# Performance work log

Hardware: AMD Instinct MI355X
Metric: run time of the kernel (lower is better)

The kernel has to match this reference:

```python
import jax, jax.numpy as jnp
import numpy as np

B, T, IN = 8, 1000, 80
CONV = 256
CCEP = 222            # ltv_out_channels
FFT_SIZE = 1024
HOP = 256
WIN = 2 * HOP         # 512
PAD = (FFT_SIZE - CCEP) // 2   # 401
NFFT = 2048


def _conv1d_same(x, W, b, groups):
    # x: (B,T,C); W: (O, C//groups, 3); equivalent to torch Conv1d pad=2 then [1:-1]
    y = jax.lax.conv_general_dilated(
        jnp.transpose(x, (0, 2, 1)), W, (1,), [(1, 1)],
        feature_group_count=groups,
        dimension_numbers=('NCH', 'OIH', 'NCH'))
    return jnp.transpose(y, (0, 2, 1)) + b


def _forward(x, z, W1, b1, W2, b2, W3, b3, W4, b4):
    Bx, Tx, _ = x.shape
    # ---- ConvLayers ----
    h = jax.nn.relu(_conv1d_same(x, W1, b1, 1))
    h = jax.nn.relu(_conv1d_same(h, W2, b2, 8))
    h = jax.nn.relu(_conv1d_same(h, W3, b3, 8))
    ccep = _conv1d_same(h, W4, b4, 1)            # (B,T,222)
    q = jnp.arange(1, CCEP // 2 + 1, dtype=x.dtype)
    quef = jnp.concatenate([q[::-1], q])          # [111..1,1..111]
    ccep = ccep / quef
    # ---- ccep -> impulse (log-magnitude cepstrum -> minimum-ish phase impulse) ----
    c = jnp.pad(ccep, ((0, 0), (0, 0), (PAD, PAD)))           # (B,T,1024)
    Y = jnp.fft.fft(c, n=FFT_SIZE, axis=-1)
    mag = jnp.power(10.0, Y.real)
    imp = jnp.fft.ifft(mag * jnp.exp(1j * Y.imag), n=FFT_SIZE, axis=-1).real  # (B,T,1024)
    # ---- time-varying impulse convolution (cross-correlation per frame) ----
    L = z.shape[-1]
    zz = z.reshape(Bx, 1, L)
    zp = jnp.pad(zz, ((0, 0), (0, 0), (WIN // 2 - 1, WIN // 2)))
    starts = jnp.arange(Tx) * HOP
    frames = zp[:, :, starts[:, None] + jnp.arange(WIN)]       # (B,1,T,512)
    fp = jnp.pad(frames, ((0, 0), (0, 0), (0, 0), (FFT_SIZE // 2 - 1, FFT_SIZE // 2)))  # len 1535
    # corr[s] = sum_k fp[s+k] * imp[k], s in [0,512); linear corr via zero-padded FFT
    Fz = jnp.fft.rfft(fp, n=NFFT, axis=-1)                     # (B,1,T,NFFT//2+1)
    Fy = jnp.fft.rfft(imp, n=NFFT, axis=-1)[:, None]           # (B,1,T,NFFT//2+1)
    corr = jnp.fft.irfft(Fz * jnp.conj(Fy), n=NFFT, axis=-1)[..., :WIN]  # (B,1,T,512)
    # ---- overlap-add ----
    n = jnp.arange(WIN, dtype=x.dtype)
    win = 0.5 * (1.0 - jnp.cos(2.0 * jnp.pi * n / WIN))        # periodic hann, win_norm=1
    zw = corr * win
    l, r = zw[..., :HOP], zw[..., HOP:]
    out = l + jnp.roll(r, 1, axis=2)
    return out.reshape(Bx, 1, Tx * HOP)


def setup_inputs() -> dict:
    key = jax.random.key(0)
    ks = jax.random.split(key, 12)
    x = jax.random.normal(ks[0], (B, T, IN), dtype=jnp.float32)
    z = jax.random.normal(ks[1], (B, 1, T * HOP), dtype=jnp.float32)
    def w(k, o, i, kk, scale):
        return jax.random.normal(k, (o, i, kk), dtype=jnp.float32) * (scale / np.sqrt(i * kk))
    W1 = w(ks[2], CONV, IN, 3, 1.0)
    b1 = jnp.zeros((CONV,), jnp.float32)
    W2 = w(ks[3], CONV, CONV // 8, 3, 1.0)
    b2 = jnp.zeros((CONV,), jnp.float32)
    W3 = w(ks[4], CONV, CONV // 8, 3, 1.0)
    b3 = jnp.zeros((CONV,), jnp.float32)
    W4 = w(ks[5], CCEP, CONV, 3, 0.01)   # small scale keeps 10**(.) well-conditioned
    b4 = jnp.zeros((CCEP,), jnp.float32)
    return {"x": x, "z": z, "W1": W1, "b1": b1, "W2": W2, "b2": b2,
            "W3": W3, "b3": b3, "W4": W4, "b4": b4}


def reference(x, z, W1, b1, W2, b2, W3, b3, W4, b4):
    return _forward(x, z, W1, b1, W2, b2, W3, b3, W4, b4)
```

## Files before the change

kernel.cpp:

```cpp
#include <hip/hip_runtime.h>
#include <hip/hip_bf16.h>

#define T_LEN 1000
#define B_N 8
#define IN_CH 80
#define CONV_CH 256
#define CCEP_N 222

typedef short s8v __attribute__((ext_vector_type(8)));
typedef _Float16 h8v __attribute__((ext_vector_type(8)));
typedef float f16v __attribute__((ext_vector_type(16)));

#define TWO_PI 6.28318530717958647692f

__global__ __launch_bounds__(256) void k_prep(
    const float* __restrict__ x,
    const float* __restrict__ W1, const float* __restrict__ W2,
    const float* __restrict__ W3, const float* __restrict__ W4,
    _Float16* __restrict__ xf, _Float16* __restrict__ W1p,
    _Float16* __restrict__ W2p, _Float16* __restrict__ W3p,
    __hip_bfloat16* __restrict__ Wc, float2* __restrict__ twTab,
    float* __restrict__ winTab) {
  const int bid = blockIdx.x, tid = threadIdx.x;
  if (bid < 3000) {
    int e = bid * 256 + tid;
    int r = e / 96, c = e - r * 96;
    xf[e] = (c < IN_CH) ? (_Float16)x[r * IN_CH + c] : (_Float16)0.f;
  } else if (bid < 3288) {
    int e = (bid - 3000) * 256 + tid;
    int kloc = e & 31, n = (e >> 5) & 255, chg = e >> 13;
    int k = chg * 32 + kloc;
    int kappa = k / 96, i = k - kappa * 96;
    W1p[e] = (i < IN_CH) ? (_Float16)W1[n * 240 + i * 3 + kappa] : (_Float16)0.f;
  } else if (bid < 3384) {
    int e = (bid - 3288) * 256 + tid;
    int kloc = e & 31, n = (e >> 5) & 255, chg = e >> 13;
    int k = chg * 32 + kloc;
    int kappa = k >> 5, iloc = k & 31;
    W2p[e] = (_Float16)W2[n * 96 + iloc * 3 + kappa];
  } else if (bid < 3480) {
    int e = (bid - 3384) * 256 + tid;
    int kloc = e & 31, n = (e >> 5) & 255, chg = e >> 13;
    int k = chg * 32 + kloc;
    int kappa = k >> 5, iloc = k & 31;
    W3p[e] = (_Float16)W3[n * 96 + iloc * 3 + kappa];
  } else if (bid < 4248) {
    int e = (bid - 3480) * 256 + tid;
    int kloc = e & 31, n = (e >> 5) & 255, chg = e >> 13;
    int kp = chg * 32 + kloc;
    int kappa = kp >> 8, i = kp & 255;
    float v = 0.f;
    if (n < CCEP_N) {
      float invq = 1.f / (float)((n < 111) ? (111 - n) : (n - 110));
      v = W4[n * 768 + i * 3 + kappa] * invq;
    }
    Wc[e] = __float2bfloat16(v);
  } else {
    int e = (bid - 4248) * 256 + tid;
    if (e < 1020) {
      int Q, off;
      if (e < 768)       { Q = 256; off = 0; }
      else if (e < 960)  { Q = 64;  off = 768; }
      else if (e < 1008) { Q = 16;  off = 960; }
      else               { Q = 4;   off = 1008; }
      int rem = e - off;
      int r = rem / Q, pos = rem - r * Q;
      float ang = (TWO_PI * (float)((r + 1) * pos)) / (float)(4 * Q);
      float s, c;
      sincosf(ang, &s, &c);
      twTab[e] = make_float2(c, s);
    } else if (e < 1532) {
      int n = e - 1020;
      winTab[n] = (0.5f - 0.5f * cosf(TWO_PI * (float)n / 512.f)) * (1.f / 1024.f);
    }
  }
}

template <int NCHG, bool GROUPED, int ACH, int APH, bool OUTBF>
__global__ __launch_bounds__(256) void k_cgemm(
    const _Float16* __restrict__ A, const _Float16* __restrict__ Bp,
    const float* __restrict__ bias, void* __restrict__ outp) {
  const int mb = blockIdx.x, b = blockIdx.y, z = blockIdx.z;
  const int t0 = mb * 32;
  const int tid = threadIdx.x;
  const int w = tid >> 6, lane = tid & 63;
  const int lm = lane & 31, half = lane >> 5;

  __shared__ _Float16 As[34 * APH];
  __shared__ _Float16 Bs[2][128 * 40];

  constexpr int ACOLS = GROUPED ? 128 : ACH;
  constexpr int NCH4 = ACOLS / 4;
  for (int e = tid; e < 34 * NCH4; e += 256) {
    int rr = e / NCH4, c4 = e - rr * NCH4;
    int t = t0 - 1 + rr;
    uint2 v = make_uint2(0u, 0u);
    if (t >= 0 && t < T_LEN)
      v = *((const uint2*)(A + (size_t)(b * T_LEN + t) * ACH +
                           (GROUPED ? z * 128 : 0)) + c4);
    *(uint2*)(As + rr * APH + c4 * 4) = v;
  }
  {
    const _Float16* src = Bp + z * 4096;
    for (int e = tid; e < 512; e += 256) {
      int nl = e >> 2, c4 = e & 3;
      *(uint4*)(Bs[0] + nl * 40 + c4 * 8) = *(const uint4*)(src + nl * 32 + c4 * 8);
    }
  }
  __syncthreads();

  f16v acc = {};
#pragma unroll
  for (int chg = 0; chg < NCHG; ++chg) {
    const int p = chg & 1;
    if (chg + 1 < NCHG) {
      const _Float16* src = Bp + (size_t)(chg + 1) * 8192 + z * 4096;
      for (int e = tid; e < 512; e += 256) {
        int nl = e >> 2, c4 = e & 3;
        *(uint4*)(Bs[p ^ 1] + nl * 40 + c4 * 8) = *(const uint4*)(src + nl * 32 + c4 * 8);
      }
    }
#pragma unroll
    for (int s = 0; s < 2; ++s) {
      const int c16 = chg * 2 + s;
      int kappa, icol;
      if constexpr (GROUPED) { kappa = c16 >> 1; icol = w * 32 + (c16 & 1) * 16; }
      else                   { kappa = c16 / 6; icol = (c16 - (c16 / 6) * 6) * 16; }
      h8v a  = *(const h8v*)(As + (lm + kappa) * APH + icol + half * 8);
      h8v bf = *(const h8v*)(Bs[p] + (w * 32 + lm) * 40 + s * 16 + half * 8);
      acc = __builtin_amdgcn_mfma_f32_32x32x16_f16(a, bf, acc, 0, 0, 0);
    }
    __syncthreads();
  }

  const int c = z * 128 + w * 32 + lm;
  const float bv = bias[c];
#pragma unroll
  for (int reg = 0; reg < 16; ++reg) {
    int row = (reg & 3) + 8 * (reg >> 2) + 4 * half;
    int t = t0 + row;
    if (t < T_LEN) {
      float v = fmaxf(acc[reg] + bv, 0.f);
      size_t idx = (size_t)(b * T_LEN + t) * CONV_CH + c;
      if constexpr (OUTBF) ((__hip_bfloat16*)outp)[idx] = __float2bfloat16(v);
      else                 ((_Float16*)outp)[idx] = (_Float16)v;
    }
  }
}

#define APITCH 264
#define BPITCH 40
#define PSTRIDE 1792000
__global__ __launch_bounds__(256) void k_conv4m(
    const __hip_bfloat16* __restrict__ h3, const __hip_bfloat16* __restrict__ Wc,
    const float* __restrict__ bias, float* __restrict__ Pbase) {
  const int mb = blockIdx.x, b = blockIdx.y, ks = blockIdx.z;
  float* __restrict__ P = Pbase + (size_t)ks * PSTRIDE;
  const int t0 = mb * 64;
  const int tid = threadIdx.x;
  const int w = tid >> 6, lane = tid & 63;
  const int wm = w >> 1, wn = w & 1;
  const int lm = lane & 31, half = lane >> 5;

  __shared__ short h3s[67 * APITCH];
  __shared__ short Bs[2][256 * BPITCH];

  const ushort* h3u = (const ushort*)h3;
  for (int g = tid; g < 67 * 64; g += 256) {
    int rr = g >> 6, c4 = g & 63;
    int t = t0 + rr - 1;
    uint2 v = make_uint2(0u, 0u);
    if (t >= 0 && t < T_LEN)
      v = *(const uint2*)(h3u + (b * T_LEN + t) * CONV_CH + c4 * 4);
    *(uint2*)(h3s + rr * APITCH + c4 * 4) = v;
  }

  const ushort* Wu = (const ushort*)(Wc) + (size_t)(ks * 6) * 8192;
#pragma unroll
  for (int it = 0; it < 4; ++it) {
    int idx = (it * 256 + tid) * 8;
    uint4 v = *(const uint4*)(Wu + idx);
    int n = idx >> 5, kloc = idx & 31;
    *(uint4*)(Bs[0] + n * BPITCH + kloc) = v;
  }
  __syncthreads();

  f16v acc0 = {}, acc1 = {}, acc2 = {}, acc3 = {};

  for (int ch = 0; ch < 6; ++ch) {
    const int p = ch & 1;
    if (ch < 5) {
      const ushort* src = Wu + (ch + 1) * 8192;
#pragma unroll
      for (int it = 0; it < 4; ++it) {
        int idx = (it * 256 + tid) * 8;
        uint4 v = *(const uint4*)(src + idx);
        int n = idx >> 5, kloc = idx & 31;
        *(uint4*)(Bs[p ^ 1] + n * BPITCH + kloc) = v;
      }
    }
#pragma unroll
    for (int s = 0; s < 2; ++s) {
      int k0 = ks * 192 + ch * 32 + s * 16;
      int kappa = k0 >> 8, i0 = k0 & 255;
      s8v a = *(const s8v*)(h3s + (wm * 32 + lm + kappa) * APITCH + i0 + half * 8);
      const short* bp = Bs[p] + (wn * 128 + lm) * BPITCH + s * 16 + half * 8;
      s8v b0 = *(const s8v*)(bp);
      s8v b1 = *(const s8v*)(bp + 32 * BPITCH);
      s8v b2 = *(const s8v*)(bp + 64 * BPITCH);
      s8v b3 = *(const s8v*)(bp + 96 * BPITCH);
      acc0 = __builtin_amdgcn_mfma_f32_32x32x16_bf16(a, b0, acc0, 0, 0, 0);
      acc1 = __builtin_amdgcn_mfma_f32_32x32x16_bf16(a, b1, acc1, 0, 0, 0);
      acc2 = __builtin_amdgcn_mfma_f32_32x32x16_bf16(a, b2, acc2, 0, 0, 0);
      acc3 = __builtin_amdgcn_mfma_f32_32x32x16_bf16(a, b3, acc3, 0, 0, 0);
    }
    __syncthreads();
  }

  const int col = lm;
#pragma unroll
  for (int nt = 0; nt < 4; ++nt) {
    int c = wn * 128 + nt * 32 + col;
    if (c >= CCEP_N) continue;
    float bq = 0.f;
    if (ks == 0) {
      float invq = 1.f / (float)((c < 111) ? (111 - c) : (c - 110));
      bq = bias[c] * invq;
    }
    const f16v* A = (nt == 0) ? &acc0 : (nt == 1) ? &acc1 : (nt == 2) ? &acc2 : &acc3;
#pragma unroll
    for (int reg = 0; reg < 16; ++reg) {
      int row = (reg & 3) + 8 * (reg >> 2) + 4 * half;
      int t = t0 + wm * 32 + row;
      if (t < T_LEN)
        P[(size_t)(b * T_LEN + t) * 224 + c] = (*A)[reg] + bq;
    }
  }
}

__device__ __forceinline__ float2 cmul(float2 a, float2 b) {
  return make_float2(fmaf(a.x, b.x, -(a.y * b.y)), fmaf(a.x, b.y, a.y * b.x));
}
__device__ __forceinline__ float2 cadd(float2 a, float2 b) { return make_float2(a.x + b.x, a.y + b.y); }
__device__ __forceinline__ float2 csub(float2 a, float2 b) { return make_float2(a.x - b.x, a.y - b.y); }

#define LIDX(i) ((i) + ((i) >> 2))

template <int Q, int OFF>
__device__ __forceinline__ void fwd_stage2(float2* __restrict__ A,
    float2* __restrict__ B, const float2* __restrict__ Tw, int j) {
  const int pos = j & (Q - 1);
  const int base = ((j - pos) << 2) + pos;
  float2 e1 = Tw[OFF + pos], e2 = Tw[OFF + Q + pos], e3 = Tw[OFF + 2 * Q + pos];
  const float2 w1 = make_float2(e1.x, -e1.y);
  const float2 w2 = make_float2(e2.x, -e2.y);
  const float2 w3 = make_float2(e3.x, -e3.y);
#pragma unroll
  for (int arr = 0; arr < 2; ++arr) {
    float2* X = arr ? B : A;
    float2 a = X[LIDX(base)], b = X[LIDX(base + Q)];
    float2 cc = X[LIDX(base + 2 * Q)], d = X[LIDX(base + 3 * Q)];
    float2 t0 = cadd(a, cc), t1 = csub(a, cc), t2 = cadd(b, d), bd = csub(b, d);
    float2 t3 = make_float2(bd.y, -bd.x);
    X[LIDX(base)]         = cadd(t0, t2);
    X[LIDX(base + Q)]     = cmul(cadd(t1, t3), w1);
    X[LIDX(base + 2 * Q)] = cmul(csub(t0, t2), w2);
    X[LIDX(base + 3 * Q)] = cmul(csub(t1, t3), w3);
  }
}

template <int Q, int OFF>
__device__ __forceinline__ void inv_stage_t(float2* __restrict__ X,
    const float2* __restrict__ Tw, int j) {
  const int pos = j & (Q - 1);
  const int base = ((j - pos) << 2) + pos;
  const float2 w1 = Tw[OFF + pos];
  const float2 w2 = Tw[OFF + Q + pos];
  const float2 w3 = Tw[OFF + 2 * Q + pos];
  float2 a = X[LIDX(base)];
  float2 b = cmul(X[LIDX(base + Q)], w1);
  float2 cc = cmul(X[LIDX(base + 2 * Q)], w2);
  float2 d = cmul(X[LIDX(base + 3 * Q)], w3);
  float2 t0 = cadd(a, cc), t1 = csub(a, cc), t2 = cadd(b, d), bd = csub(b, d);
  float2 t3 = make_float2(-bd.y, bd.x);
  X[LIDX(base)]         = cadd(t0, t2);
  X[LIDX(base + Q)]     = cadd(t1, t3);
  X[LIDX(base + 2 * Q)] = csub(t0, t2);
  X[LIDX(base + 3 * Q)] = csub(t1, t3);
}

__device__ __forceinline__ int rev4d(int v) {
  return ((v & 3) << 6) | (((v >> 2) & 3) << 4) | (((v >> 4) & 3) << 2) | ((v >> 6) & 3);
}

__global__ __launch_bounds__(256) void k_fft(const float* __restrict__ Pb,
    const float* __restrict__ z, const float2* __restrict__ twg,
    const float* __restrict__ wing, float* __restrict__ out,
    float* __restrict__ sbl, float* __restrict__ sbr) {
  const int u = blockIdx.x, b = blockIdx.y;
  const int tA = 2 * u, tB = tA + 1;
  const int btA = b * T_LEN + tA, btB = btA + 1;
  const int j = threadIdx.x;
  __shared__ float2 WlA[1280];
  __shared__ float2 WlB[1280];
  __shared__ float2 Tws[1020];
  for (int e = j; e < 1020; e += 256) Tws[e] = twg[e];

  const float* zb = z + b * 256000;
  float f0A = 0.f, fS, f1B = 0.f;
  {
    int zi0 = tA * 256 + j - 255;
    f0A = (zi0 >= 0) ? zb[zi0] : 0.f;
    fS = zb[tA * 256 + j + 1];
    int zi2 = tB * 256 + j + 1;
    f1B = (zi2 < 256000) ? zb[zi2] : 0.f;
  }
  float c1A = 0.f, c2A = 0.f, c1B = 0.f, c2B = 0.f;
  if (j >= 145) {
    int mA = btA * 224 + (j - 145), mB = btB * 224 + (j - 145);
    c1A = (Pb[mA] + Pb[mA + PSTRIDE]) + (Pb[mA + 2 * PSTRIDE] + Pb[mA + 3 * PSTRIDE]);
    c1B = (Pb[mB] + Pb[mB + PSTRIDE]) + (Pb[mB + 2 * PSTRIDE] + Pb[mB + 3 * PSTRIDE]);
  }
  if (j < 111) {
    int mA = btA * 224 + (j + 111), mB = btB * 224 + (j + 111);
    c2A = (Pb[mA] + Pb[mA + PSTRIDE]) + (Pb[mA + 2 * PSTRIDE] + Pb[mA + 3 * PSTRIDE]);
    c2B = (Pb[mB] + Pb[mB + PSTRIDE]) + (Pb[mB + 2 * PSTRIDE] + Pb[mB + 3 * PSTRIDE]);
  }
  __syncthreads();

  {
    float2 e1 = Tws[j], e2 = Tws[256 + j], e3 = Tws[512 + j];
    const float2 w1 = make_float2(e1.x, -e1.y);
    const float2 w2 = make_float2(e2.x, -e2.y);
    const float2 w3 = make_float2(e3.x, -e3.y);
    {
      float2 t0 = make_float2(c2A, f0A);
      float2 t1 = make_float2(-c2A, f0A);
      float2 t2 = make_float2(c1A, fS);
      float2 t3 = make_float2(fS, -c1A);
      WlA[LIDX(j)]       = cadd(t0, t2);
      WlA[LIDX(j + 256)] = cmul(cadd(t1, t3), w1);
      WlA[LIDX(j + 512)] = cmul(csub(t0, t2), w2);
      WlA[LIDX(j + 768)] = cmul(csub(t1, t3), w3);
    }
    {
      float2 t0 = make_float2(c2B, fS);
      float2 t1 = make_float2(-c2B, fS);
      float2 t2 = make_float2(c1B, f1B);
      float2 t3 = make_float2(f1B, -c1B);
      WlB[LIDX(j)]       = cadd(t0, t2);
      WlB[LIDX(j + 256)] = cmul(cadd(t1, t3), w1);
      WlB[LIDX(j + 512)] = cmul(csub(t0, t2), w2);
      WlB[LIDX(j + 768)] = cmul(csub(t1, t3), w3);
    }
  }
  __syncthreads();

  fwd_stage2<64, 768>(WlA, WlB, Tws, j);  __syncthreads();
  fwd_stage2<16, 960>(WlA, WlB, Tws, j);  __syncthreads();
  fwd_stage2<4, 1008>(WlA, WlB, Tws, j);  __syncthreads();

  const int base = 4 * j;
  float2 XA[4], XB[4];
  {
    float2 u0 = WlA[LIDX(base)], u1 = WlA[LIDX(base + 1)];
    float2 u2 = WlA[LIDX(base + 2)], u3 = WlA[LIDX(base + 3)];
    float2 t0 = cadd(u0, u2), t1 = csub(u0, u2), t2 = cadd(u1, u3), bd = csub(u1, u3);
    float2 t3 = make_float2(bd.y, -bd.x);
    XA[0] = cadd(t0, t2); XA[1] = cadd(t1, t3); XA[2] = csub(t0, t2); XA[3] = csub(t1, t3);
  }
  {
    float2 u0 = WlB[LIDX(base)], u1 = WlB[LIDX(base + 1)];
    float2 u2 = WlB[LIDX(base + 2)], u3 = WlB[LIDX(base + 3)];
    float2 t0 = cadd(u0, u2), t1 = csub(u0, u2), t2 = cadd(u1, u3), bd = csub(u1, u3);
    float2 t3 = make_float2(bd.y, -bd.x);
    XB[0] = cadd(t0, t2); XB[1] = cadd(t1, t3); XB[2] = csub(t0, t2); XB[3] = csub(t1, t3);
  }
#pragma unroll
  for (int q = 0; q < 4; ++q) { WlA[LIDX(base + q)] = XA[q]; WlB[LIDX(base + q)] = XB[q]; }
  __syncthreads();

  const int r0 = rev4d(j);
  const bool self0 = (r0 == 0);
  const int jp = self0 ? 0 : rev4d((256 - r0) & 255);
  float2 PA[4], PB[4];
#pragma unroll
  for (int q = 0; q < 4; ++q) { PA[q] = WlA[LIDX(4 * jp + q)]; PB[q] = WlB[LIDX(4 * jp + q)]; }
  float2 Z[4];
#pragma unroll
  for (int q = 0; q < 4; ++q) {
    float2 SA, SB;
    {
      float2 A = XA[q];
      float2 Bc = self0 ? PA[(4 - q) & 3] : PA[3 - q];
      float2 Y = make_float2(0.5f * (A.x + Bc.x), 0.5f * (A.y - Bc.y));
      float2 F = make_float2(0.5f * (A.y + Bc.y), -0.5f * (A.x - Bc.x));
      float mag = __expf(Y.x * 2.30258509299404568402f);
      float sy, cy;
      __sincosf(Y.y, &sy, &cy);
      float gr = mag * cy, gi = mag * sy;
      SA = make_float2(fmaf(F.x, gr, F.y * gi), fmaf(F.x, gi, -(F.y * gr)));
    }
    {
      float2 A = XB[q];
      float2 Bc = self0 ? PB[(4 - q) & 3] : PB[3 - q];
      float2 Y = make_float2(0.5f * (A.x + Bc.x), 0.5f * (A.y - Bc.y));
      float2 F = make_float2(0.5f * (A.y + Bc.y), -0.5f * (A.x - Bc.x));
      float mag = __expf(Y.x * 2.30258509299404568402f);
      float sy, cy;
      __sincosf(Y.y, &sy, &cy);
      float gr = mag * cy, gi = mag * sy;
      SB = make_float2(fmaf(F.x, gr, F.y * gi), fmaf(F.x, gi, -(F.y * gr)));
    }
    Z[q] = make_float2(SA.x - SB.y, SA.y + SB.x);
  }
  __syncthreads();

  {
    float2 t0 = cadd(Z[0], Z[2]), t1 = csub(Z[0], Z[2]), t2 = cadd(Z[1], Z[3]), bd = csub(Z[1], Z[3]);
    float2 t3 = make_float2(-bd.y, bd.x);
    WlA[LIDX(base)]     = cadd(t0, t2);
    WlA[LIDX(base + 1)] = cadd(t1, t3);
    WlA[LIDX(base + 2)] = csub(t0, t2);
    WlA[LIDX(base + 3)] = csub(t1, t3);
  }
  __syncthreads();

  inv_stage_t<4, 1008>(WlA, Tws, j);  __syncthreads();
  inv_stage_t<16, 960>(WlA, Tws, j);  __syncthreads();
  inv_stage_t<64, 768>(WlA, Tws, j);  __syncthreads();

  {
    float2 w1 = Tws[j], w2 = Tws[256 + j], w3 = Tws[512 + j];
    float2 a = WlA[LIDX(j)];
    float2 bb = cmul(WlA[LIDX(j + 256)], w1);
    float2 cc = cmul(WlA[LIDX(j + 512)], w2);
    float2 d = cmul(WlA[LIDX(j + 768)], w3);
    float2 t0 = cadd(a, cc), t1 = csub(a, cc), t2 = cadd(bb, d), bd = csub(bb, d);
    float2 t3 = make_float2(-bd.y, bd.x);
    float2 Cj    = cadd(t0, t2);
    float2 Cj256 = cadd(t1, t3);
    int n1 = 511 - j, n2 = 255 - j;
    float wn1 = wing[n1], wn2 = wing[n2];
    float vA_l = Cj256.x * wn2;
    float vAB  = Cj.x * wn1 + Cj256.y * wn2;
    float vB_r = Cj.y * wn1;
    out[(b * T_LEN + tB) * 256 + n2] = vAB;
    int su = (b * 500 + u) * 256 + n2;
    sbl[su] = vA_l;
    sbr[su] = vB_r;
  }
}

__global__ __launch_bounds__(256) void k_even(const float* __restrict__ sbl,
    const float* __restrict__ sbr, float* __restrict__ out) {
  int idx = blockIdx.x * 256 + threadIdx.x;
  int n = idx & 255;
  int bu = idx >> 8;
  int u = bu % 500, b = bu / 500;
  int up = (u == 0) ? 499 : u - 1;
  out[(b * T_LEN + 2 * u) * 256 + n] = sbl[idx] + sbr[(b * 500 + up) * 256 + n];
}

extern "C" void kernel_launch(void* const* d_in, const int* in_sizes, int n_in,
                              void* d_out, int out_size, void* d_ws, size_t ws_size,
                              hipStream_t stream) {
  const float* x  = (const float*)d_in[0];
  const float* z  = (const float*)d_in[1];
  const float* W1 = (const float*)d_in[2];
  const float* b1 = (const float*)d_in[3];
  const float* W2 = (const float*)d_in[4];
  const float* b2 = (const float*)d_in[5];
  const float* W3 = (const float*)d_in[6];
  const float* b3 = (const float*)d_in[7];
  const float* W4 = (const float*)d_in[8];
  const float* b4 = (const float*)d_in[9];

  float* ws   = (float*)d_ws;
  __hip_bfloat16* h3bf = (__hip_bfloat16*)ws;
  float* Pb   = ws + 1024000;
  float* sbl  = ws + 8192000;
  float* sbr  = ws + 9216000;
  _Float16* W1p = (_Float16*)(ws + 10240000);
  _Float16* W2p = (_Float16*)(ws + 10301440);
  _Float16* W3p = (_Float16*)(ws + 10326016);
  __hip_bfloat16* Wc = (__hip_bfloat16*)(ws + 10350592);
  float2* twTab = (float2*)(ws + 10448896);
  float* winTab = ws + 10450944;
  _Float16* xf16 = (_Float16*)(ws + 10451456);
  _Float16* h1f = (_Float16*)sbl;
  _Float16* h2f = (_Float16*)sbr;
  float* out = (float*)d_out;

  dim3 blk(256);
  k_prep<<<4254, blk, 0, stream>>>(x, W1, W2, W3, W4, xf16, W1p, W2p, W3p,
                                   Wc, twTab, winTab);

  dim3 gc(32, B_N, 2);
  k_cgemm<9, false, 96, 104, false><<<gc, blk, 0, stream>>>(xf16, W1p, b1, (void*)h1f);
  k_cgemm<3, true, 256, 136, false><<<gc, blk, 0, stream>>>(h1f, W2p, b2, (void*)h2f);
  k_cgemm<3, true, 256, 136, true><<<gc, blk, 0, stream>>>(h2f, W3p, b3, (void*)h3bf);
  dim3 g4(16, B_N, 4);
  k_conv4m<<<g4, blk, 0, stream>>>(h3bf, Wc, b4, Pb);
  dim3 gf(T_LEN / 2, B_N);
  k_fft<<<gf, blk, 0, stream>>>(Pb, z, twTab, winTab, out, sbl, sbr);
  k_even<<<4000, blk, 0, stream>>>(sbl, sbr, out);
}
```

Baseline: 158.0 us.

## Fuse three conv layers into one kernel with halo recompute in LDS

Replaces the three separate conv GEMM launches with one kernel that keeps the h1 and h2 intermediates in shared memory. Each block recomputes a few halo timesteps (36 and 34 rows) so the following layers can run without going back to global memory. The fp32-to-fp16 conversion of x also moves into the fused kernel, which removes that pass from k_prep. This saves two launches and the global write and read-back of h1 and h2, at the cost of some extra MFMA work for the halo rows and higher LDS use per block.

```diff
diff --git a/kernel.cpp b/kernel.cpp
--- a/kernel.cpp
+++ b/kernel.cpp
@@ -14,38 +14,33 @@
 #define TWO_PI 6.28318530717958647692f
 
 __global__ __launch_bounds__(256) void k_prep(
-    const float* __restrict__ x,
     const float* __restrict__ W1, const float* __restrict__ W2,
     const float* __restrict__ W3, const float* __restrict__ W4,
-    _Float16* __restrict__ xf, _Float16* __restrict__ W1p,
-    _Float16* __restrict__ W2p, _Float16* __restrict__ W3p,
+    _Float16* __restrict__ W1p, _Float16* __restrict__ W2p,
+    _Float16* __restrict__ W3p,
     __hip_bfloat16* __restrict__ Wc, float2* __restrict__ twTab,
     float* __restrict__ winTab) {
   const int bid = blockIdx.x, tid = threadIdx.x;
-  if (bid < 3000) {
+  if (bid < 288) {
     int e = bid * 256 + tid;
-    int r = e / 96, c = e - r * 96;
-    xf[e] = (c < IN_CH) ? (_Float16)x[r * IN_CH + c] : (_Float16)0.f;
-  } else if (bid < 3288) {
-    int e = (bid - 3000) * 256 + tid;
     int kloc = e & 31, n = (e >> 5) & 255, chg = e >> 13;
     int k = chg * 32 + kloc;
     int kappa = k / 96, i = k - kappa * 96;
     W1p[e] = (i < IN_CH) ? (_Float16)W1[n * 240 + i * 3 + kappa] : (_Float16)0.f;
-  } else if (bid < 3384) {
-    int e = (bid - 3288) * 256 + tid;
+  } else if (bid < 384) {
+    int e = (bid - 288) * 256 + tid;
     int kloc = e & 31, n = (e >> 5) & 255, chg = e >> 13;
     int k = chg * 32 + kloc;
     int kappa = k >> 5, iloc = k & 31;
     W2p[e] = (_Float16)W2[n * 96 + iloc * 3 + kappa];
-  } else if (bid < 3480) {
-    int e = (bid - 3384) * 256 + tid;
+  } else if (bid < 480) {
+    int e = (bid - 384) * 256 + tid;
     int kloc = e & 31, n = (e >> 5) & 255, chg = e >> 13;
     int k = chg * 32 + kloc;
     int kappa = k >> 5, iloc = k & 31;
     W3p[e] = (_Float16)W3[n * 96 + iloc * 3 + kappa];
-  } else if (bid < 4248) {
-    int e = (bid - 3480) * 256 + tid;
+  } else if (bid < 1248) {
+    int e = (bid - 480) * 256 + tid;
     int kloc = e & 31, n = (e >> 5) & 255, chg = e >> 13;
     int kp = chg * 32 + kloc;
     int kappa = kp >> 8, i = kp & 255;
@@ -56,7 +51,7 @@
     }
     Wc[e] = __float2bfloat16(v);
   } else {
-    int e = (bid - 4248) * 256 + tid;
+    int e = (bid - 1248) * 256 + tid;
     if (e < 1020) {
       int Q, off;
       if (e < 768)       { Q = 256; off = 0; }
@@ -76,74 +71,173 @@
   }
 }
 
-template <int NCHG, bool GROUPED, int ACH, int APH, bool OUTBF>
-__global__ __launch_bounds__(256) void k_cgemm(
-    const _Float16* __restrict__ A, const _Float16* __restrict__ Bp,
-    const float* __restrict__ bias, void* __restrict__ outp) {
+#define XP2 112
+#define HP2 144
+#define BP2 48
+
+__global__ __launch_bounds__(256) void k_convfused(
+    const float* __restrict__ x,
+    const _Float16* __restrict__ W1p, const float* __restrict__ b1,
+    const _Float16* __restrict__ W2p, const float* __restrict__ b2,
+    const _Float16* __restrict__ W3p, const float* __restrict__ b3,
+    __hip_bfloat16* __restrict__ out) {
   const int mb = blockIdx.x, b = blockIdx.y, z = blockIdx.z;
   const int t0 = mb * 32;
   const int tid = threadIdx.x;
   const int w = tid >> 6, lane = tid & 63;
   const int lm = lane & 31, half = lane >> 5;
-
-  __shared__ _Float16 As[34 * APH];
-  __shared__ _Float16 Bs[2][128 * 40];
-
-  constexpr int ACOLS = GROUPED ? 128 : ACH;
-  constexpr int NCH4 = ACOLS / 4;
-  for (int e = tid; e < 34 * NCH4; e += 256) {
-    int rr = e / NCH4, c4 = e - rr * NCH4;
-    int t = t0 - 1 + rr;
-    uint2 v = make_uint2(0u, 0u);
-    if (t >= 0 && t < T_LEN)
-      v = *((const uint2*)(A + (size_t)(b * T_LEN + t) * ACH +
-                           (GROUPED ? z * 128 : 0)) + c4);
-    *(uint2*)(As + rr * APH + c4 * 4) = v;
-  }
-  {
-    const _Float16* src = Bp + z * 4096;
+  const int n0loc = w * 32;
+  const int c = z * 128 + n0loc + lm;
+
+  __shared__ _Float16 xs[38 * XP2];
+  __shared__ _Float16 h1s[36 * HP2];
+  __shared__ _Float16 h2s[34 * HP2];
+  __shared__ _Float16 Bs[2][128 * BP2];
+
+  for (int e = tid; e < 38 * 96; e += 256) {
+    int rr = e / 96, cc = e - rr * 96;
+    int t = t0 - 3 + rr;
+    float v = (cc < IN_CH && t >= 0 && t < T_LEN)
+                  ? x[(b * T_LEN + t) * IN_CH + cc] : 0.f;
+    xs[rr * XP2 + cc] = (_Float16)v;
+  }
+  {
+    const _Float16* src = W1p + z * 4096;
     for (int e = tid; e < 512; e += 256) {
       int nl = e >> 2, c4 = e & 3;
-      *(uint4*)(Bs[0] + nl * 40 + c4 * 8) = *(const uint4*)(src + nl * 32 + c4 * 8);
-    }
-  }
-  __syncthreads();
-
-  f16v acc = {};
-#pragma unroll
-  for (int chg = 0; chg < NCHG; ++chg) {
-    const int p = chg & 1;
-    if (chg + 1 < NCHG) {
-      const _Float16* src = Bp + (size_t)(chg + 1) * 8192 + z * 4096;
-      for (int e = tid; e < 512; e += 256) {
-        int nl = e >> 2, c4 = e & 3;
-        *(uint4*)(Bs[p ^ 1] + nl * 40 + c4 * 8) = *(const uint4*)(src + nl * 32 + c4 * 8);
-      }
-    }
-#pragma unroll
-    for (int s = 0; s < 2; ++s) {
-      const int c16 = chg * 2 + s;
-      int kappa, icol;
-      if constexpr (GROUPED) { kappa = c16 >> 1; icol = w * 32 + (c16 & 1) * 16; }
-      else                   { kappa = c16 / 6; icol = (c16 - (c16 / 6) * 6) * 16; }
-      h8v a  = *(const h8v*)(As + (lm + kappa) * APH + icol + half * 8);
-      h8v bf = *(const h8v*)(Bs[p] + (w * 32 + lm) * 40 + s * 16 + half * 8);
-      acc = __builtin_amdgcn_mfma_f32_32x32x16_f16(a, bf, acc, 0, 0, 0);
-    }
-    __syncthreads();
-  }
-
-  const int c = z * 128 + w * 32 + lm;
-  const float bv = bias[c];
-#pragma unroll
-  for (int reg = 0; reg < 16; ++reg) {
-    int row = (reg & 3) + 8 * (reg >> 2) + 4 * half;
-    int t = t0 + row;
-    if (t < T_LEN) {
-      float v = fmaxf(acc[reg] + bv, 0.f);
-      size_t idx = (size_t)(b * T_LEN + t) * CONV_CH + c;
-      if constexpr (OUTBF) ((__hip_bfloat16*)outp)[idx] = __float2bfloat16(v);
-      else                 ((_Float16*)outp)[idx] = (_Float16)v;
+      *(uint4*)(Bs[0] + nl * BP2 + c4 * 8) = *(const uint4*)(src + nl * 32 + c4 * 8);
+    }
+  }
+  __syncthreads();
+
+  {
+    f16v a0 = {}, a1 = {};
+    for (int chg = 0; chg < 9; ++chg) {
+      const int p = chg & 1;
+      if (chg + 1 < 9) {
+        const _Float16* src = W1p + (size_t)(chg + 1) * 8192 + z * 4096;
+        for (int e = tid; e < 512; e += 256) {
+          int nl = e >> 2, c4 = e & 3;
+          *(uint4*)(Bs[p ^ 1] + nl * BP2 + c4 * 8) = *(const uint4*)(src + nl * 32 + c4 * 8);
+        }
+      }
+#pragma unroll
+      for (int s = 0; s < 2; ++s) {
+        const int c16 = chg * 2 + s;
+        const int kappa = c16 / 6;
+        const int icol = (c16 - kappa * 6) * 16;
+        h8v bf = *(const h8v*)(Bs[p] + (n0loc + lm) * BP2 + s * 16 + half * 8);
+        h8v aa0 = *(const h8v*)(xs + (lm + kappa) * XP2 + icol + half * 8);
+        h8v aa1 = *(const h8v*)(xs + (lm + kappa + 4) * XP2 + icol + half * 8);
+        a0 = __builtin_amdgcn_mfma_f32_32x32x16_f16(aa0, bf, a0, 0, 0, 0);
+        a1 = __builtin_amdgcn_mfma_f32_32x32x16_f16(aa1, bf, a1, 0, 0, 0);
+      }
+      __syncthreads();
+    }
+    const float bv = b1[c];
+#pragma unroll
+    for (int reg = 0; reg < 16; ++reg) {
+      int row = (reg & 3) + 8 * (reg >> 2) + 4 * half;
+      {
+        int t = t0 - 2 + row;
+        float v = (t >= 0 && t < T_LEN) ? fmaxf(a0[reg] + bv, 0.f) : 0.f;
+        h1s[row * HP2 + n0loc + lm] = (_Float16)v;
+      }
+      if (row >= 28) {
+        int t = t0 + 2 + row;
+        float v = (t >= 0 && t < T_LEN) ? fmaxf(a1[reg] + bv, 0.f) : 0.f;
+        h1s[(row + 4) * HP2 + n0loc + lm] = (_Float16)v;
+      }
+    }
+  }
+  {
+    const _Float16* src = W2p + z * 4096;
+    for (int e = tid; e < 512; e += 256) {
+      int nl = e >> 2, c4 = e & 3;
+      *(uint4*)(Bs[0] + nl * BP2 + c4 * 8) = *(const uint4*)(src + nl * 32 + c4 * 8);
+    }
+  }
+  __syncthreads();
+
+  {
+    f16v a0 = {}, a1 = {};
+    for (int chg = 0; chg < 3; ++chg) {
+      const int p = chg & 1;
+      if (chg + 1 < 3) {
+        const _Float16* src = W2p + (size_t)(chg + 1) * 8192 + z * 4096;
+        for (int e = tid; e < 512; e += 256) {
+          int nl = e >> 2, c4 = e & 3;
+          *(uint4*)(Bs[p ^ 1] + nl * BP2 + c4 * 8) = *(const uint4*)(src + nl * 32 + c4 * 8);
+        }
+      }
+#pragma unroll
+      for (int s = 0; s < 2; ++s) {
+        const int c16 = chg * 2 + s;
+        const int kappa = c16 >> 1;
+        const int icol = n0loc + (c16 & 1) * 16;
+        h8v bf = *(const h8v*)(Bs[p] + (n0loc + lm) * BP2 + s * 16 + half * 8);
+        h8v aa0 = *(const h8v*)(h1s + (lm + kappa) * HP2 + icol + half * 8);
+        h8v aa1 = *(const h8v*)(h1s + (lm + kappa + 2) * HP2 + icol + half * 8);
+        a0 = __builtin_amdgcn_mfma_f32_32x32x16_f16(aa0, bf, a0, 0, 0, 0);
+        a1 = __builtin_amdgcn_mfma_f32_32x32x16_f16(aa1, bf, a1, 0, 0, 0);
+      }
+      __syncthreads();
+    }
+    const float bv = b2[c];
+#pragma unroll
+    for (int reg = 0; reg < 16; ++reg) {
+      int row = (reg & 3) + 8 * (reg >> 2) + 4 * half;
+      {
+        int t = t0 - 1 + row;
+        float v = (t >= 0 && t < T_LEN) ? fmaxf(a0[reg] + bv, 0.f) : 0.f;
+        h2s[row * HP2 + n0loc + lm] = (_Float16)v;
+      }
+      if (row >= 30) {
+        int t = t0 + 1 + row;
+        float v = (t >= 0 && t < T_LEN) ? fmaxf(a1[reg] + bv, 0.f) : 0.f;
+        h2s[(row + 2) * HP2 + n0loc + lm] = (_Float16)v;
+      }
+    }
+  }
+  {
+    const _Float16* src = W3p + z * 4096;
+    for (int e = tid; e < 512; e += 256) {
+      int nl = e >> 2, c4 = e & 3;
+      *(uint4*)(Bs[0] + nl * BP2 + c4 * 8) = *(const uint4*)(src + nl * 32 + c4 * 8);
+    }
+  }
+  __syncthreads();
+
+  {
+    f16v a0 = {};
+    for (int chg = 0; chg < 3; ++chg) {
+      const int p = chg & 1;
+      if (chg + 1 < 3) {
+        const _Float16* src = W3p + (size_t)(chg + 1) * 8192 + z * 4096;
+        for (int e = tid; e < 512; e += 256) {
+          int nl = e >> 2, c4 = e & 3;
+          *(uint4*)(Bs[p ^ 1] + nl * BP2 + c4 * 8) = *(const uint4*)(src + nl * 32 + c4 * 8);
+        }
+      }
+#pragma unroll
+      for (int s = 0; s < 2; ++s) {
+        const int c16 = chg * 2 + s;
+        const int kappa = c16 >> 1;
+        const int icol = n0loc + (c16 & 1) * 16;
+        h8v bf = *(const h8v*)(Bs[p] + (n0loc + lm) * BP2 + s * 16 + half * 8);
+        h8v aa = *(const h8v*)(h2s + (lm + kappa) * HP2 + icol + half * 8);
+        a0 = __builtin_amdgcn_mfma_f32_32x32x16_f16(aa, bf, a0, 0, 0, 0);
+      }
+      __syncthreads();
+    }
+    const float bv = b3[c];
+#pragma unroll
+    for (int reg = 0; reg < 16; ++reg) {
+      int row = (reg & 3) + 8 * (reg >> 2) + 4 * half;
+      int t = t0 + row;
+      if (t < T_LEN)
+        out[(size_t)(b * T_LEN + t) * CONV_CH + c] =
+            __float2bfloat16(fmaxf(a0[reg] + bv, 0.f));
     }
   }
 }
@@ -487,19 +581,14 @@
   __hip_bfloat16* Wc = (__hip_bfloat16*)(ws + 10350592);
   float2* twTab = (float2*)(ws + 10448896);
   float* winTab = ws + 10450944;
-  _Float16* xf16 = (_Float16*)(ws + 10451456);
-  _Float16* h1f = (_Float16*)sbl;
-  _Float16* h2f = (_Float16*)sbr;
   float* out = (float*)d_out;
 
   dim3 blk(256);
-  k_prep<<<4254, blk, 0, stream>>>(x, W1, W2, W3, W4, xf16, W1p, W2p, W3p,
+  k_prep<<<1254, blk, 0, stream>>>(W1, W2, W3, W4, W1p, W2p, W3p,
                                    Wc, twTab, winTab);
 
   dim3 gc(32, B_N, 2);
-  k_cgemm<9, false, 96, 104, false><<<gc, blk, 0, stream>>>(xf16, W1p, b1, (void*)h1f);
-  k_cgemm<3, true, 256, 136, false><<<gc, blk, 0, stream>>>(h1f, W2p, b2, (void*)h2f);
-  k_cgemm<3, true, 256, 136, true><<<gc, blk, 0, stream>>>(h2f, W3p, b3, (void*)h3bf);
+  k_convfused<<<gc, blk, 0, stream>>>(x, W1p, b1, W2p, b2, W3p, b3, h3bf);
   dim3 g4(16, B_N, 4);
   k_conv4m<<<g4, blk, 0, stream>>>(h3bf, Wc, b4, Pb);
   dim3 gf(T_LEN / 2, B_N);
```

Measured after the change: 150.4 us. 4.8% less time.
